# Kernel tuning notes

Measured on AMD Instinct MI355X. Metric: run time of the kernel, lower is better.

## Reference

```python
import jax, jax.numpy as jnp
import numpy as np

NUM_BATCH = 8  # GroupNormalization(num_batch=num_groups) with num_groups=8
EPS = 1e-6


def setup_inputs() -> dict:
    key = jax.random.key(0)
    k1, k2, k3 = jax.random.split(key, 3)
    b, h, w, c = 32, 32, 32, 256
    x = jax.random.normal(k1, (b, h, w, c), dtype=jnp.float32)
    gamma = jnp.ones((c,), dtype=jnp.float32)
    beta = jnp.zeros((c,), dtype=jnp.float32)
    w_qkv = jax.random.normal(k2, (c, 3 * c), dtype=jnp.float32) * 0.02
    w_out = jax.random.normal(k3, (c, c), dtype=jnp.float32) * 0.02
    return {"x": x, "gamma": gamma, "beta": beta, "w_qkv": w_qkv, "w_out": w_out}


def reference(x, gamma, beta, w_qkv, w_out):
    b, h, w, c = x.shape
    # --- GroupNormalization (exact quirky semantics of the source) ---
    # num_groups = c // num_batch; reshape to [-1, num_groups, group_size]
    # -> per-(b,h,w)-pixel normalization over contiguous channel groups.
    ng = c // NUM_BATCH          # 32 groups
    gs = c // ng                 # 8 channels per group
    g = x.reshape(-1, ng, gs)
    mu = jnp.mean(g, axis=-1, keepdims=True)
    var = jnp.mean(jnp.square(g - mu), axis=-1, keepdims=True)
    xn = ((g - mu) / jnp.sqrt(var + EPS)).reshape(x.shape)
    xn = gamma * xn + beta
    # --- 1x1 conv to qkv (bias-free) ---
    qkv = jnp.einsum('bhwc,cd->bhwd', xn, w_qkv)  # [b,h,w,3c]
    q, k, v = jnp.split(qkv, 3, axis=-1)
    # self_attention=True branch: tie q=k=v to their mean
    t = (v + q + k) / 3.0
    q = k = v = t
    # --- exact reshapes from the source (raw reshapes, not transposes) ---
    q = jnp.transpose(q, (0, 3, 1, 2)).reshape(b, h * w, c)  # [b,hw,c]
    k = k.reshape(b, c, h * w)                               # [b,c,hw]
    v = jnp.transpose(v, (0, 3, 1, 2)).reshape(b, h * w, c)  # [b,hw,c]
    scores = jnp.matmul(q, k) * (c ** -0.5)                  # [b,hw,hw]
    attn = jax.nn.softmax(scores, axis=-1)
    # NOTE: source passes transpose_a=float (truthy) -> attention is transposed
    out = jnp.matmul(jnp.swapaxes(attn, 1, 2), v)            # [b,hw,c]
    out = out.reshape(b, h, w, c)
    return jnp.einsum('bhwc,cd->bhwd', out, w_out) + x
```

## Files before the change

kernel.cpp:

```cpp
#include <hip/hip_runtime.h>

typedef unsigned short u16;
typedef unsigned char u8;
typedef long long i64;
typedef __bf16 bf16x8 __attribute__((ext_vector_type(8)));
typedef float f32x4 __attribute__((ext_vector_type(4)));
typedef u16 u16x8 __attribute__((ext_vector_type(8)));

#define GLD16(g, l) __builtin_amdgcn_global_load_lds( \
    (const __attribute__((address_space(1))) void*)(g), \
    (__attribute__((address_space(3))) void*)(l), 16, 0, 0)

__device__ __forceinline__ float bf2f(u16 u) {
  return __uint_as_float(((unsigned)u) << 16);
}
__device__ __forceinline__ u16 f2bf(float f) {
  unsigned u = __float_as_uint(f);
  return (u16)((u + 0x7fffu + ((u >> 16) & 1u)) >> 16);
}
__device__ __forceinline__ u8 f8e_sw(float v) {
  unsigned u = __float_as_uint(v);
  unsigned s = (u >> 24) & 0x80u;
  u &= 0x7fffffffu;
  if (u < 0x3c000000u) return (u8)s;
  int b = (int)((u + 0x7FFFFu + ((u >> 20) & 1u)) >> 20) - 960;
  b = b < 8 ? 8 : (b > 126 ? 126 : b);
  return (u8)(b | s);
}
__device__ __forceinline__ float f8d_sw(u8 b) {
  if (!(b & 0x7f)) return 0.0f;
  float v = __uint_as_float((((unsigned)(b & 0x7fu)) << 20) + 0x3C000000u);
  return (b & 0x80u) ? -v : v;
}
__device__ __forceinline__ unsigned pk4(float a, float b, float c, float d) {
#if __has_builtin(__builtin_amdgcn_cvt_pk_fp8_f32)
  int r = __builtin_amdgcn_cvt_pk_fp8_f32(a, b, 0, false);
  r = __builtin_amdgcn_cvt_pk_fp8_f32(c, d, r, true);
  return (unsigned)r;
#else
  return (unsigned)f8e_sw(a) | ((unsigned)f8e_sw(b) << 8) |
         ((unsigned)f8e_sw(c) << 16) | ((unsigned)f8e_sw(d) << 24);
#endif
}
__device__ __forceinline__ float f8df(u8 b) {
#if __has_builtin(__builtin_amdgcn_cvt_f32_fp8)
  return __builtin_amdgcn_cvt_f32_fp8((int)b, 0);
#else
  return f8d_sw(b);
#endif
}
__device__ __forceinline__ int sig(int r) { return (r ^ (r >> 3)) & 7; }

__global__ void combine_w(const float* __restrict__ wqkv, const float* __restrict__ wout,
                          u16* __restrict__ wtT, u16* __restrict__ woutT) {
  int c = blockIdx.x, d = threadIdx.x;
  float t = (wqkv[c * 768 + d] + wqkv[c * 768 + 256 + d] + wqkv[c * 768 + 512 + d]) * (1.0f / 3.0f);
  wtT[d * 256 + c] = f2bf(t);
  woutT[d * 256 + c] = f2bf(wout[c * 256 + d]);
}

__global__ __launch_bounds__(512) void gnT(
    const float* __restrict__ x, const float* __restrict__ gamma,
    const float* __restrict__ beta, const u16* __restrict__ wtT,
    u8* __restrict__ Q8, u8* __restrict__ Kt8) {
  __shared__ u16 lA[2][64 * 64];
  __shared__ u16 lB[2][256 * 64];
  const int m0 = blockIdx.x * 64;
  const int z = m0 >> 10;
  const int t = threadIdx.x, lane = t & 63;
  const int w = t >> 6, wr = w >> 2, wc = w & 3;
  f32x4 acc[2][4] = {};

#define GNT_STAGE(B, K0)                                                        \
  {                                                                             \
    _Pragma("unroll") for (int ch = 0; ch < 4; ch++) {                          \
      int flat = ch * 512 + t, row = flat >> 3, slot = flat & 7;                \
      GLD16(wtT + (size_t)row * 256 + (K0) + (slot ^ sig(row)) * 8,             \
            lB[B] + flat * 8);                                                  \
    }                                                                           \
    int row = t >> 3, grp = t & 7;                                              \
    const float* xp = x + (size_t)(m0 + row) * 256 + (K0) + grp * 8;            \
    float4 a = *(const float4*)xp, b = *(const float4*)(xp + 4);                \
    float mu = (a.x + a.y + a.z + a.w + b.x + b.y + b.z + b.w) * 0.125f;        \
    float d0 = a.x - mu, d1 = a.y - mu, d2 = a.z - mu, d3 = a.w - mu;           \
    float d4 = b.x - mu, d5 = b.y - mu, d6 = b.z - mu, d7 = b.w - mu;           \
    float var = (d0 * d0 + d1 * d1 + d2 * d2 + d3 * d3 +                        \
                 d4 * d4 + d5 * d5 + d6 * d6 + d7 * d7) * 0.125f;               \
    float rs = rsqrtf(var + 1e-6f);                                             \
    const float4 g0 = *(const float4*)(gamma + (K0) + grp * 8);                 \
    const float4 g1 = *(const float4*)(gamma + (K0) + grp * 8 + 4);             \
    const float4 e0 = *(const float4*)(beta + (K0) + grp * 8);                  \
    const float4 e1 = *(const float4*)(beta + (K0) + grp * 8 + 4);              \
    u16x8 o;                                                                    \
    o[0] = f2bf(g0.x * (d0 * rs) + e0.x); o[1] = f2bf(g0.y * (d1 * rs) + e0.y); \
    o[2] = f2bf(g0.z * (d2 * rs) + e0.z); o[3] = f2bf(g0.w * (d3 * rs) + e0.w); \
    o[4] = f2bf(g1.x * (d4 * rs) + e1.x); o[5] = f2bf(g1.y * (d5 * rs) + e1.y); \
    o[6] = f2bf(g1.z * (d6 * rs) + e1.z); o[7] = f2bf(g1.w * (d7 * rs) + e1.w); \
    *(u16x8*)(lA[B] + row * 64 + (grp ^ sig(row)) * 8) = o;                     \
  }

  GNT_STAGE(0, 0);
  __syncthreads();
  for (int it = 0; it < 4; it++) {
    if (it < 3) { GNT_STAGE((it + 1) & 1, (it + 1) * 64); }
    const u16* la = lA[it & 1];
    const u16* lb = lB[it & 1];
#pragma unroll
    for (int kk = 0; kk < 2; kk++) {
      bf16x8 af[2], bfr[4];
#pragma unroll
      for (int mi = 0; mi < 2; mi++) {
        int m = wr * 32 + mi * 16 + (lane & 15);
        af[mi] = *(const bf16x8*)(la + m * 64 + ((kk * 32 + (lane >> 4) * 8) ^ (sig(m) << 3)));
      }
#pragma unroll
      for (int ni = 0; ni < 4; ni++) {
        int n = wc * 64 + ni * 16 + (lane & 15);
        bfr[ni] = *(const bf16x8*)(lb + n * 64 + ((kk * 32 + (lane >> 4) * 8) ^ (sig(n) << 3)));
      }
#pragma unroll
      for (int mi = 0; mi < 2; mi++)
#pragma unroll
        for (int ni = 0; ni < 4; ni++)
          acc[mi][ni] = __builtin_amdgcn_mfma_f32_16x16x32_bf16(af[mi], bfr[ni], acc[mi][ni], 0, 0, 0);
    }
    __syncthreads();
  }

  const int rb = m0 + wr * 32 + ((lane >> 4) << 2);
  const int cb = wc * 64 + (lane & 15);
  u8* kt = (u8*)lB[0];
  u8* qtile = (u8*)lB[1];
#pragma unroll
  for (int mi = 0; mi < 2; mi++)
#pragma unroll
    for (int ni = 0; ni < 4; ni++) {
      int P0 = rb + mi * 16, c = cb + ni * 16;
      int pl = P0 - m0;
      unsigned pk = pk4(acc[mi][ni][0], acc[mi][ni][1], acc[mi][ni][2], acc[mi][ni][3]);
#pragma unroll
      for (int j = 0; j < 4; j++)
        kt[(j * 256 + c) * 16 + (pl >> 2)] = (u8)(pk >> (8 * j));
      *(unsigned*)(qtile + c * 80 + pl) = pk;
    }
  __syncthreads();
  const int ckb = (m0 & 1023) >> 2;
  u8* Kz = Kt8 + (size_t)z * 262144;
  u8* Qz = Q8 + (size_t)z * 262144;
#pragma unroll
  for (int r2 = 0; r2 < 2; r2++) {
    int r = t * 2 + r2;
    uint4 v = *(const uint4*)(kt + r * 16);
    *(uint4*)(Kz + (size_t)r * 256 + ckb) = v;
  }
#pragma unroll
  for (int ph = 0; ph < 2; ph++) {
    int idx = ph * 512 + t, c = idx >> 2, q = idx & 3;
    uint4 v = *(const uint4*)(qtile + c * 80 + q * 16);
    *(uint4*)(Qz + (size_t)c * 1024 + (m0 & 1023) + q * 16) = v;
  }
#undef GNT_STAGE
}

__global__ __launch_bounds__(256) void gemm_s8(
    const u8* __restrict__ Q8, const u8* __restrict__ Kt8,
    u8* __restrict__ Et, float* __restrict__ partials) {
  __shared__ u8 lA[128 * 256];
  __shared__ u8 lB[128 * 256];
  const int z = blockIdx.z;
  const u8* Az = Q8 + (size_t)z * 262144;
  const u8* Bz = Kt8 + (size_t)z * 262144;
  u8* Ez = Et + (size_t)z * 1048576;
  const int m0 = blockIdx.x * 128, n0 = blockIdx.y * 128;
  const int t = threadIdx.x, lane = t & 63;
  const int wr = (t >> 6) >> 1, wc = (t >> 6) & 1;
  f32x4 acc[4][4] = {};

#pragma unroll
  for (int ch = 0; ch < 8; ch++) {
    int flat = ch * 256 + t, row = flat >> 4, slot = flat & 15;
    GLD16(Az + (size_t)(m0 + row) * 256 + (slot ^ sig(row)) * 16, lA + flat * 16);
  }
#pragma unroll
  for (int ch = 0; ch < 8; ch++) {
    int flat = ch * 256 + t, row = flat >> 4, slot = flat & 15;
    GLD16(Bz + (size_t)(n0 + row) * 256 + (slot ^ sig(row)) * 16, lB + flat * 16);
  }
  __syncthreads();
#pragma unroll
  for (int kk = 0; kk < 8; kk++) {
    i64 af[4], bfv[4];
    int koff = kk * 32 + (lane >> 4) * 8;
#pragma unroll
    for (int mi = 0; mi < 4; mi++) {
      int m = wr * 64 + mi * 16 + (lane & 15);
      af[mi] = *(const i64*)(lA + m * 256 + (koff ^ (sig(m) << 4)));
    }
#pragma unroll
    for (int ni = 0; ni < 4; ni++) {
      int n = wc * 64 + ni * 16 + (lane & 15);
      bfv[ni] = *(const i64*)(lB + n * 256 + (koff ^ (sig(n) << 4)));
    }
#pragma unroll
    for (int mi = 0; mi < 4; mi++)
#pragma unroll
      for (int ni = 0; ni < 4; ni++)
        acc[mi][ni] = __builtin_amdgcn_mfma_f32_16x16x32_fp8_fp8(af[mi], bfv[ni], acc[mi][ni], 0, 0, 0);
  }
  __syncthreads();
  u8* ldsC = lA;
  const int rbl = wr * 64 + ((lane >> 4) << 2);
  const int cbl = wc * 64 + (lane & 15);
  const float SCL = 0.0625f * 1.44269504089f;
  float ps[4][4] = {};
#pragma unroll
  for (int mi = 0; mi < 4; mi++)
#pragma unroll
    for (int ni = 0; ni < 4; ni++) {
      int pl = cbl + ni * 16, ib = rbl + mi * 16;
      float e0 = exp2f(acc[mi][ni][0] * SCL);
      float e1 = exp2f(acc[mi][ni][1] * SCL);
      float e2 = exp2f(acc[mi][ni][2] * SCL);
      float e3 = exp2f(acc[mi][ni][3] * SCL);
      ps[mi][0] += e0; ps[mi][1] += e1; ps[mi][2] += e2; ps[mi][3] += e3;
      *(unsigned*)(ldsC + pl * 128 + (ib ^ ((pl & 7) << 4))) = pk4(e0, e1, e2, e3);
    }
#pragma unroll
  for (int mi = 0; mi < 4; mi++)
#pragma unroll
    for (int j = 0; j < 4; j++) {
      float v = ps[mi][j];
      v += __shfl_xor(v, 1); v += __shfl_xor(v, 2);
      v += __shfl_xor(v, 4); v += __shfl_xor(v, 8);
      if ((lane & 15) == 0)
        partials[(size_t)(z * 1024 + m0 + rbl + mi * 16 + j) * 16 + blockIdx.y * 2 + wc] = v;
    }
  __syncthreads();
#pragma unroll
  for (int ph = 0; ph < 4; ph++) {
    int pl = ph * 32 + (t >> 3), ich = (t & 7) * 16;
    uint4 v = *(const uint4*)(ldsC + pl * 128 + (ich ^ ((pl & 7) << 4)));
    *(uint4*)(Ez + (size_t)(n0 + pl) * 1024 + m0 + ich) = v;
  }
}

__global__ __launch_bounds__(256) void qt8(
    const u8* __restrict__ Q8, const float* __restrict__ partials, u8* __restrict__ Qt) {
  __shared__ u8 tile[64][260];
  __shared__ float rv[64];
  const int z = blockIdx.y, i0 = blockIdx.x * 64;
  const u8* src = Q8 + (size_t)z * 262144;
  u8* dst = Qt + (size_t)z * 262144;
  const int t = threadIdx.x;
#pragma unroll
  for (int q = 0; q < 4; q++) {
    uint4 v = *(const uint4*)(src + (size_t)(i0 + (t >> 2)) * 256 + (t & 3) * 64 + q * 16);
    *(uint4*)(&tile[t >> 2][(t & 3) * 64 + q * 16]) = v;
  }
  if (t < 64) {
    const float4* p = (const float4*)(partials + (size_t)(z * 1024 + i0 + t) * 16);
    float4 a = p[0], b = p[1], c = p[2], d = p[3];
    float s = ((a.x + a.y) + (a.z + a.w)) + ((b.x + b.y) + (b.z + b.w)) +
              ((c.x + c.y) + (c.z + c.w)) + ((d.x + d.y) + (d.z + d.w));
    rv[t] = 1024.0f / s;
  }
  __syncthreads();
#pragma unroll
  for (int q = 0; q < 4; q++) {
    unsigned wd[4];
#pragma unroll
    for (int d = 0; d < 4; d++) {
      float f[4];
#pragma unroll
      for (int e = 0; e < 4; e++) {
        int i = q * 16 + d * 4 + e;
        f[e] = f8df(tile[i][t]) * rv[i];
      }
      wd[d] = pk4(f[0], f[1], f[2], f[3]);
    }
    uint4 v = {wd[0], wd[1], wd[2], wd[3]};
    *(uint4*)(dst + (size_t)t * 1024 + i0 + q * 16) = v;
  }
}

__global__ __launch_bounds__(512) void gemm_o8(
    const u8* __restrict__ Et, const u8* __restrict__ Qt, u16* __restrict__ ob) {
  __shared__ u8 lA[2][128 * 128];
  __shared__ u8 lB[2][256 * 128];
  const int z = blockIdx.z;
  const u8* Az = Et + (size_t)z * 1048576;
  const u8* Bz = Qt + (size_t)z * 262144;
  const int m0 = blockIdx.x * 128;
  const int t = threadIdx.x, lane = t & 63;
  const int w = t >> 6, wr = w >> 2, wc = w & 3;
  f32x4 acc[4][4] = {};

#define O8_STAGE(B, K0)                                                       \
  {                                                                           \
    _Pragma("unroll") for (int ch = 0; ch < 2; ch++) {                        \
      int flat = ch * 512 + t, row = flat >> 3, slot = flat & 7;              \
      GLD16(Az + (size_t)(m0 + row) * 1024 + (K0) + (slot ^ sig(row)) * 16,   \
            lA[B] + flat * 16);                                               \
    }                                                                         \
    _Pragma("unroll") for (int ch = 0; ch < 4; ch++) {                        \
      int flat = ch * 512 + t, row = flat >> 3, slot = flat & 7;              \
      GLD16(Bz + (size_t)row * 1024 + (K0) + (slot ^ sig(row)) * 16,          \
            lB[B] + flat * 16);                                               \
    }                                                                         \
  }

  O8_STAGE(0, 0);
  __syncthreads();
  for (int it = 0; it < 8; it++) {
    if (it < 7) { O8_STAGE((it + 1) & 1, (it + 1) * 128); }
    const u8* la = lA[it & 1];
    const u8* lb = lB[it & 1];
#pragma unroll
    for (int kk = 0; kk < 4; kk++) {
      i64 af[4], bfv[4];
      int koff = kk * 32 + (lane >> 4) * 8;
#pragma unroll
      for (int mi = 0; mi < 4; mi++) {
        int m = wr * 64 + mi * 16 + (lane & 15);
        af[mi] = *(const i64*)(la + m * 128 + (koff ^ (sig(m) << 4)));
      }
#pragma unroll
      for (int ni = 0; ni < 4; ni++) {
        int n = wc * 64 + ni * 16 + (lane & 15);
        bfv[ni] = *(const i64*)(lb + n * 128 + (koff ^ (sig(n) << 4)));
      }
#pragma unroll
      for (int mi = 0; mi < 4; mi++)
#pragma unroll
        for (int ni = 0; ni < 4; ni++)
          acc[mi][ni] = __builtin_amdgcn_mfma_f32_16x16x32_fp8_fp8(af[mi], bfv[ni], acc[mi][ni], 0, 0, 0);
    }
    __syncthreads();
  }
  const int rb = m0 + wr * 64 + ((lane >> 4) << 2);
  const int cb = wc * 64 + (lane & 15);
#pragma unroll
  for (int mi = 0; mi < 4; mi++)
#pragma unroll
    for (int ni = 0; ni < 4; ni++)
#pragma unroll
      for (int j = 0; j < 4; j++)
        ob[(size_t)(z * 1024 + rb + mi * 16 + j) * 256 + cb + ni * 16] =
            f2bf(acc[mi][ni][j] * (1.0f / 1024.0f));
#undef O8_STAGE
}

__global__ __launch_bounds__(512) void gemm_f(
    const u16* __restrict__ A, const u16* __restrict__ woutT,
    const float* __restrict__ x, float* __restrict__ C) {
  __shared__ u16 lA[2][64 * 64];
  __shared__ u16 lB[2][256 * 64];
  const int m0 = blockIdx.x * 64;
  const int t = threadIdx.x, lane = t & 63;
  const int w = t >> 6, wr = w >> 2, wc = w & 3;
  f32x4 acc[2][4] = {};

#define F_STAGE(B, K0)                                                        \
  {                                                                           \
    int row = t >> 3, slot = t & 7;                                           \
    GLD16(A + (size_t)(m0 + row) * 256 + (K0) + (slot ^ sig(row)) * 8,        \
          lA[B] + t * 8);                                                     \
    _Pragma("unroll") for (int ch = 0; ch < 4; ch++) {                        \
      int flat = ch * 512 + t, r2 = flat >> 3, s2 = flat & 7;                 \
      GLD16(woutT + (size_t)r2 * 256 + (K0) + (s2 ^ sig(r2)) * 8,             \
            lB[B] + flat * 8);                                                \
    }                                                                         \
  }

  F_STAGE(0, 0);
  __syncthreads();
  for (int it = 0; it < 4; it++) {
    if (it < 3) { F_STAGE((it + 1) & 1, (it + 1) * 64); }
    const u16* la = lA[it & 1];
    const u16* lb = lB[it & 1];
#pragma unroll
    for (int kk = 0; kk < 2; kk++) {
      bf16x8 af[2], bfr[4];
#pragma unroll
      for (int mi = 0; mi < 2; mi++) {
        int m = wr * 32 + mi * 16 + (lane & 15);
        af[mi] = *(const bf16x8*)(la + m * 64 + ((kk * 32 + (lane >> 4) * 8) ^ (sig(m) << 3)));
      }
#pragma unroll
      for (int ni = 0; ni < 4; ni++) {
        int n = wc * 64 + ni * 16 + (lane & 15);
        bfr[ni] = *(const bf16x8*)(lb + n * 64 + ((kk * 32 + (lane >> 4) * 8) ^ (sig(n) << 3)));
      }
#pragma unroll
      for (int mi = 0; mi < 2; mi++)
#pragma unroll
        for (int ni = 0; ni < 4; ni++)
          acc[mi][ni] = __builtin_amdgcn_mfma_f32_16x16x32_bf16(af[mi], bfr[ni], acc[mi][ni], 0, 0, 0);
    }
    __syncthreads();
  }
  const int rb = m0 + wr * 32 + ((lane >> 4) << 2);
  const int cb = wc * 64 + (lane & 15);
#pragma unroll
  for (int mi = 0; mi < 2; mi++)
#pragma unroll
    for (int ni = 0; ni < 4; ni++)
#pragma unroll
      for (int j = 0; j < 4; j++) {
        size_t idx = (size_t)(rb + mi * 16 + j) * 256 + cb + ni * 16;
        C[idx] = acc[mi][ni][j] + x[idx];
      }
#undef F_STAGE
}

extern "C" void kernel_launch(void* const* d_in, const int* in_sizes, int n_in,
                              void* d_out, int out_size, void* d_ws, size_t ws_size,
                              hipStream_t stream) {
  (void)in_sizes; (void)n_in; (void)out_size; (void)ws_size;
  const float* x = (const float*)d_in[0];
  const float* gamma = (const float*)d_in[1];
  const float* beta = (const float*)d_in[2];
  const float* wqkv = (const float*)d_in[3];
  const float* wout = (const float*)d_in[4];
  float* outp = (float*)d_out;

  char* ws = (char*)d_ws;
  const size_t MB = 1024 * 1024;
  u16* wtT = (u16*)(ws + 0);
  u16* woutT = (u16*)(ws + (128 << 10));
  float* partials = (float*)(ws + (512 << 10));
  u8* Q8 = (u8*)(ws + 3 * MB);
  u8* Kt8 = (u8*)(ws + 12 * MB);
  u8* Qt = (u8*)(ws + 21 * MB);
  u8* Et = (u8*)(ws + 30 * MB);
  u16* ob = (u16*)(ws + 63 * MB);

  combine_w<<<256, 256, 0, stream>>>(wqkv, wout, wtT, woutT);
  gnT<<<512, 512, 0, stream>>>(x, gamma, beta, wtT, Q8, Kt8);
  gemm_s8<<<dim3(8, 8, 32), 256, 0, stream>>>(Q8, Kt8, Et, partials);
  qt8<<<dim3(16, 32), 256, 0, stream>>>(Q8, partials, Qt);
  gemm_o8<<<dim3(8, 1, 32), 512, 0, stream>>>(Et, Qt, ob);
  gemm_f<<<512, 512, 0, stream>>>(ob, woutT, x, outp);
}
```

Measured before the change: 102.0 us.

## Fuse attention-output GEMM with output projection and residual add

Merges the fp8 attention-output GEMM and the bf16 w_out projection into one kernel. The 128x256 bf16 attention tile stays in swizzled LDS and is multiplied directly by staged w_out tiles. This removes the intermediate global buffer round trip and one kernel launch. In exchange it uses 128KB of LDS per block, which limits occupancy to one block per CU, and the second GEMM runs on only 256 blocks instead of 512.

```diff
diff --git a/kernel.cpp b/kernel.cpp
--- a/kernel.cpp
+++ b/kernel.cpp
@@ -283,11 +283,12 @@
   }
 }
 
-__global__ __launch_bounds__(512) void gemm_o8(
-    const u8* __restrict__ Et, const u8* __restrict__ Qt, u16* __restrict__ ob) {
-  __shared__ u8 lA[2][128 * 128];
-  __shared__ u8 lB[2][256 * 128];
-  const int z = blockIdx.z;
+__global__ __launch_bounds__(512) void gemm_of(
+    const u8* __restrict__ Et, const u8* __restrict__ Qt,
+    const u16* __restrict__ woutT, const float* __restrict__ x,
+    float* __restrict__ C) {
+  __shared__ char smem[131072];
+  const int z = blockIdx.y;
   const u8* Az = Et + (size_t)z * 1048576;
   const u8* Bz = Qt + (size_t)z * 262144;
   const int m0 = blockIdx.x * 128;
@@ -297,15 +298,17 @@
 
 #define O8_STAGE(B, K0)                                                       \
   {                                                                           \
+    u8* la_ = (u8*)smem + (B) * 16384;                                        \
+    u8* lb_ = (u8*)smem + 32768 + (B) * 32768;                                \
     _Pragma("unroll") for (int ch = 0; ch < 2; ch++) {                        \
       int flat = ch * 512 + t, row = flat >> 3, slot = flat & 7;              \
       GLD16(Az + (size_t)(m0 + row) * 1024 + (K0) + (slot ^ sig(row)) * 16,   \
-            lA[B] + flat * 16);                                               \
+            la_ + flat * 16);                                                 \
     }                                                                         \
     _Pragma("unroll") for (int ch = 0; ch < 4; ch++) {                        \
       int flat = ch * 512 + t, row = flat >> 3, slot = flat & 7;              \
       GLD16(Bz + (size_t)row * 1024 + (K0) + (slot ^ sig(row)) * 16,          \
-            lB[B] + flat * 16);                                               \
+            lb_ + flat * 16);                                                 \
     }                                                                         \
   }
 
@@ -313,8 +316,8 @@
   __syncthreads();
   for (int it = 0; it < 8; it++) {
     if (it < 7) { O8_STAGE((it + 1) & 1, (it + 1) * 128); }
-    const u8* la = lA[it & 1];
-    const u8* lb = lB[it & 1];
+    const u8* la = (const u8*)smem + (it & 1) * 16384;
+    const u8* lb = (const u8*)smem + 32768 + (it & 1) * 32768;
 #pragma unroll
     for (int kk = 0; kk < 4; kk++) {
       i64 af[4], bfv[4];
@@ -337,54 +340,46 @@
     }
     __syncthreads();
   }
-  const int rb = m0 + wr * 64 + ((lane >> 4) << 2);
-  const int cb = wc * 64 + (lane & 15);
-#pragma unroll
-  for (int mi = 0; mi < 4; mi++)
-#pragma unroll
-    for (int ni = 0; ni < 4; ni++)
-#pragma unroll
-      for (int j = 0; j < 4; j++)
-        ob[(size_t)(z * 1024 + rb + mi * 16 + j) * 256 + cb + ni * 16] =
-            f2bf(acc[mi][ni][j] * (1.0f / 1024.0f));
 #undef O8_STAGE
-}
-
-__global__ __launch_bounds__(512) void gemm_f(
-    const u16* __restrict__ A, const u16* __restrict__ woutT,
-    const float* __restrict__ x, float* __restrict__ C) {
-  __shared__ u16 lA[2][64 * 64];
-  __shared__ u16 lB[2][256 * 64];
-  const int m0 = blockIdx.x * 64;
-  const int t = threadIdx.x, lane = t & 63;
-  const int w = t >> 6, wr = w >> 2, wc = w & 3;
-  f32x4 acc[2][4] = {};
-
-#define F_STAGE(B, K0)                                                        \
+
+#define W_STAGE(B, K0)                                                        \
   {                                                                           \
-    int row = t >> 3, slot = t & 7;                                           \
-    GLD16(A + (size_t)(m0 + row) * 256 + (K0) + (slot ^ sig(row)) * 8,        \
-          lA[B] + t * 8);                                                     \
+    u16* wb_ = (u16*)(smem + 65536 + (B) * 32768);                            \
     _Pragma("unroll") for (int ch = 0; ch < 4; ch++) {                        \
-      int flat = ch * 512 + t, r2 = flat >> 3, s2 = flat & 7;                 \
-      GLD16(woutT + (size_t)r2 * 256 + (K0) + (s2 ^ sig(r2)) * 8,             \
-            lB[B] + flat * 8);                                                \
+      int flat = ch * 512 + t, row = flat >> 3, slot = flat & 7;              \
+      GLD16(woutT + (size_t)row * 256 + (K0) + (slot ^ sig(row)) * 8,         \
+            (u8*)wb_ + flat * 16);                                            \
     }                                                                         \
   }
-
-  F_STAGE(0, 0);
-  __syncthreads();
-  for (int it = 0; it < 4; it++) {
-    if (it < 3) { F_STAGE((it + 1) & 1, (it + 1) * 64); }
-    const u16* la = lA[it & 1];
-    const u16* lb = lB[it & 1];
+  W_STAGE(0, 0);
+  {
+    const int rbl = wr * 64 + ((lane >> 4) << 2);
+    const int cbl = wc * 64 + (lane & 15);
+#pragma unroll
+    for (int mi = 0; mi < 4; mi++)
+#pragma unroll
+      for (int ni = 0; ni < 4; ni++)
+#pragma unroll
+        for (int j = 0; j < 4; j++) {
+          int pl = rbl + mi * 16 + j, c = cbl + ni * 16;
+          int byteoff = (pl * 512 + c * 2) ^ ((pl & 7) << 4);
+          *(u16*)(smem + byteoff) = f2bf(acc[mi][ni][j] * (1.0f / 1024.0f));
+        }
+  }
+  __syncthreads();
+
+  f32x4 acc2[4][4] = {};
+  for (int it2 = 0; it2 < 4; it2++) {
+    if (it2 < 3) { W_STAGE((it2 + 1) & 1, (it2 + 1) * 64); }
+    const u16* lb = (const u16*)(smem + 65536 + (it2 & 1) * 32768);
 #pragma unroll
     for (int kk = 0; kk < 2; kk++) {
-      bf16x8 af[2], bfr[4];
-#pragma unroll
-      for (int mi = 0; mi < 2; mi++) {
-        int m = wr * 32 + mi * 16 + (lane & 15);
-        af[mi] = *(const bf16x8*)(la + m * 64 + ((kk * 32 + (lane >> 4) * 8) ^ (sig(m) << 3)));
+      bf16x8 af[4], bfr[4];
+#pragma unroll
+      for (int mi = 0; mi < 4; mi++) {
+        int m = wr * 64 + mi * 16 + (lane & 15);
+        int kg = it2 * 64 + kk * 32 + (lane >> 4) * 8;
+        af[mi] = *(const bf16x8*)(smem + ((m * 512 + kg * 2) ^ ((m & 7) << 4)));
       }
 #pragma unroll
       for (int ni = 0; ni < 4; ni++) {
@@ -392,25 +387,26 @@
         bfr[ni] = *(const bf16x8*)(lb + n * 64 + ((kk * 32 + (lane >> 4) * 8) ^ (sig(n) << 3)));
       }
 #pragma unroll
-      for (int mi = 0; mi < 2; mi++)
+      for (int mi = 0; mi < 4; mi++)
 #pragma unroll
         for (int ni = 0; ni < 4; ni++)
-          acc[mi][ni] = __builtin_amdgcn_mfma_f32_16x16x32_bf16(af[mi], bfr[ni], acc[mi][ni], 0, 0, 0);
+          acc2[mi][ni] = __builtin_amdgcn_mfma_f32_16x16x32_bf16(af[mi], bfr[ni], acc2[mi][ni], 0, 0, 0);
     }
     __syncthreads();
   }
-  const int rb = m0 + wr * 32 + ((lane >> 4) << 2);
+#undef W_STAGE
+
+  const int Pb = z * 1024 + m0 + wr * 64 + ((lane >> 4) << 2);
   const int cb = wc * 64 + (lane & 15);
 #pragma unroll
-  for (int mi = 0; mi < 2; mi++)
+  for (int mi = 0; mi < 4; mi++)
 #pragma unroll
     for (int ni = 0; ni < 4; ni++)
 #pragma unroll
       for (int j = 0; j < 4; j++) {
-        size_t idx = (size_t)(rb + mi * 16 + j) * 256 + cb + ni * 16;
-        C[idx] = acc[mi][ni][j] + x[idx];
-      }
-#undef F_STAGE
+        size_t idx = (size_t)(Pb + mi * 16 + j) * 256 + cb + ni * 16;
+        C[idx] = acc2[mi][ni][j] + x[idx];
+      }
 }
 
 extern "C" void kernel_launch(void* const* d_in, const int* in_sizes, int n_in,
@@ -433,12 +429,10 @@
   u8* Kt8 = (u8*)(ws + 12 * MB);
   u8* Qt = (u8*)(ws + 21 * MB);
   u8* Et = (u8*)(ws + 30 * MB);
-  u16* ob = (u16*)(ws + 63 * MB);
 
   combine_w<<<256, 256, 0, stream>>>(wqkv, wout, wtT, woutT);
   gnT<<<512, 512, 0, stream>>>(x, gamma, beta, wtT, Q8, Kt8);
   gemm_s8<<<dim3(8, 8, 32), 256, 0, stream>>>(Q8, Kt8, Et, partials);
   qt8<<<dim3(16, 32), 256, 0, stream>>>(Q8, partials, Qt);
-  gemm_o8<<<dim3(8, 1, 32), 512, 0, stream>>>(Et, Qt, ob);
-  gemm_f<<<512, 512, 0, stream>>>(ob, woutT, x, outp);
-}
+  gemm_of<<<dim3(8, 32), 512, 0, stream>>>(Et, Qt, woutT, x, outp);
+}
```

After: 102.8 us. No clear change (+0.7%).
